# Optimization experiments

Hardware: AMD Instinct MI355X
Metric: run time of the kernel (lower is better)

The kernel has to match this reference:

```python
import jax, jax.numpy as jnp
import numpy as np

IN_FEATURES = 1024
OUT_FEATURES = 256
GRID_SIZE = 5
SPLINE_ORDER = 3
SCALE_BASE = 1.0
GRID_RANGE = (-1.0, 1.0)


def make_grid():
    h = (GRID_RANGE[1] - GRID_RANGE[0]) / GRID_SIZE
    g = jnp.arange(-SPLINE_ORDER, GRID_SIZE + SPLINE_ORDER + 1, dtype=jnp.float32) * h + GRID_RANGE[0]
    # (in_features, grid_size + 2*spline_order + 1) = (1024, 12)
    return jnp.broadcast_to(g[None, :], (IN_FEATURES, g.shape[0]))


def setup_inputs() -> dict:
    key = jax.random.key(0)
    k1, k2, k3 = jax.random.split(key, 3)
    batch = 16384
    x = jax.random.normal(k1, (batch, IN_FEATURES), dtype=jnp.float32)
    base_weight = jax.random.normal(k2, (OUT_FEATURES, IN_FEATURES), dtype=jnp.float32) * 0.03
    n_basis = GRID_SIZE + SPLINE_ORDER  # 8
    spline_weight = (jax.random.uniform(k3, (OUT_FEATURES, IN_FEATURES * n_basis), dtype=jnp.float32) - 0.5) * 0.1 / n_basis
    grid = make_grid()
    return {"x": x, "base_weight": base_weight, "spline_weight": spline_weight, "grid": grid}


def b_splines(x, grid):
    # x: (B, F) -> (B, F, grid_size + spline_order)
    xe = x[:, :, None]  # (B, F, 1)
    bases = ((xe >= grid[:, :-1]) & (xe < grid[:, 1:])).astype(x.dtype)
    for k in range(1, SPLINE_ORDER + 1):
        left = (xe - grid[:, : -(k + 1)]) / (grid[:, k:-1] - grid[:, : -(k + 1)])
        right = (grid[:, k + 1 :] - xe) / (grid[:, k + 1 :] - grid[:, 1:-k])
        bases = left * bases[:, :, :-1] + right * bases[:, :, 1:]
    return bases.reshape(x.shape[0], -1)  # (B, F*(grid_size+spline_order))


def reference(x, base_weight, spline_weight, grid):
    base_out = jax.nn.silu(x) @ (base_weight * SCALE_BASE).T  # (B, out)
    spline_basis = b_splines(x, grid)                          # (B, F*8)
    spline_out = spline_basis @ spline_weight.T                # (B, out)
    return base_out + spline_out
```

## Files before the change

### kernel.cpp

```cpp
#include <hip/hip_runtime.h>
#include <cstdint>
#include <cstddef>

typedef unsigned short u16;
typedef unsigned int   u32;
typedef unsigned long long u64;
typedef __attribute__((ext_vector_type(8))) short short8;
typedef __attribute__((ext_vector_type(4))) float f32x4;

#define M_ROWS 16384
#define N_COLS 256
#define IN_F   1024
#define K_SPL  8192
#define K_TOT  9216
#define NCHUNK 144
#define SPLITK 2
#define CPB    (NCHUNK / SPLITK)

__device__ __forceinline__ u32 f2bf1(float f) {
  u32 u = __float_as_uint(f);
  u += 0x7fffu + ((u >> 16) & 1u);
  return u >> 16;
}
__device__ __forceinline__ u32 pk2(float a, float b) {
  return f2bf1(a) | (f2bf1(b) << 16);
}
__device__ __forceinline__ float silu(float v) {
  return v * __builtin_amdgcn_rcpf(1.f + __expf(-v));
}

__device__ __forceinline__ uint4 basis8(float xv) {
  float u = fmaf(xv, 2.5f, 5.5f);
  int i0 = (int)u;
  float fr = u - (float)i0;
  float fr2 = fr * fr, fr3 = fr2 * fr;
  float om  = 1.f - fr;
  float om3 = om * om * om;
  float w0 = om3 * (1.f / 6.f);
  float w3 = fr3 * (1.f / 6.f);
  float w1 = fmaf(fr3, 0.5f, fmaf(fr2, -1.f, 2.f / 3.f));
  float w2 = fmaf(fr + fr2 - fr3, 0.5f, 1.f / 6.f);
  u64 W = (u64)pk2(w0, w1) | ((u64)pk2(w2, w3) << 32);
  if (!(u >= 0.f && u < 11.f)) W = 0ull;
  int s = (i0 - 3) * 16;
  u64 lo, hi;
  if (s >= 64)      { int r = s - 64; lo = 0ull; hi = (r < 64) ? (W << r) : 0ull; }
  else if (s > 0)   { lo = W << s;    hi = W >> (64 - s); }
  else if (s == 0)  { lo = W;         hi = 0ull; }
  else              { int r = -s;     lo = (r < 64) ? (W >> r) : 0ull; hi = 0ull; }
  uint4 o;
  o.x = (u32)lo; o.y = (u32)(lo >> 32); o.z = (u32)hi; o.w = (u32)(hi >> 32);
  return o;
}

__global__ void pack_weights(const float* __restrict__ bw, const float* __restrict__ sw,
                             u16* __restrict__ Bp) {
  int o  = blockIdx.y;
  int k4 = (blockIdx.x * blockDim.x + threadIdx.x) * 4;
  const float* src = (k4 < K_SPL) ? (sw + (size_t)o * K_SPL + k4)
                                  : (bw + (size_t)o * IN_F + (k4 - K_SPL));
  float a = src[0], b = src[1], c = src[2], d = src[3];
  uint2 v; v.x = pk2(a, b); v.y = pk2(c, d);
  *(uint2*)(Bp + (size_t)o * K_TOT + k4) = v;
}

__global__ __launch_bounds__(512, 4)
void kan_gemm(const float* __restrict__ x, const u16* __restrict__ Bp,
              float* __restrict__ out) {
  __shared__ __align__(16) u16 Bs[2 * 256 * 64];
  __shared__ __align__(16) u16 As[2 * 64 * 64];

  const int tid  = threadIdx.x;
  const int lane = tid & 63;
  const int w    = tid >> 6;
  const int wm   = w & 1;
  const int wn   = w >> 1;

  const int bid  = blockIdx.x;
  const int kid  = bid & 1;
  const int mb   = bid >> 1;
  const int row0 = mb * 64;
  const int cs   = kid * CPB, c1 = cs + CPB;

  f32x4 acc[2][4];
#pragma unroll
  for (int i = 0; i < 2; ++i)
#pragma unroll
    for (int j = 0; j < 4; ++j)
      acc[i][j] = (f32x4){0.f, 0.f, 0.f, 0.f};

  const int sr = tid >> 3;
  const int sq = tid & 7;

  const int lm = lane & 15;
  const int kg = lane >> 4;
  int a_off[2][2], b_off[2][4];
#pragma unroll
  for (int h = 0; h < 2; ++h) {
    int c = h * 4 + kg;
#pragma unroll
    for (int i = 0; i < 2; ++i) {
      int ra = wm * 32 + i * 16 + lm;
      a_off[h][i] = ra * 64 + ((c ^ (ra & 7)) * 8);
    }
#pragma unroll
    for (int j = 0; j < 4; ++j) {
      int rb = wn * 64 + j * 16 + lm;
      b_off[h][j] = rb * 64 + ((c ^ (rb & 7)) * 8);
    }
  }

  float px;
  float4 pb0, pb1;

  auto LOADX = [&](int c) {
    if (c < 128) {
      px = x[(size_t)(row0 + sr) * IN_F + c * 8 + sq];
    } else {
      const float* xp = x + (size_t)(row0 + sr) * IN_F + (c - 128) * 64 + sq * 8;
      pb0 = *(const float4*)xp;
      pb1 = *(const float4*)(xp + 4);
    }
  };

  auto BUILD = [&](int c, int buf) {
    uint4 q;
    if (c < 128) {
      q = basis8(px);
    } else {
      q.x = pk2(silu(pb0.x), silu(pb0.y));
      q.y = pk2(silu(pb0.z), silu(pb0.w));
      q.z = pk2(silu(pb1.x), silu(pb1.y));
      q.w = pk2(silu(pb1.z), silu(pb1.w));
    }
    *(uint4*)(As + buf * (64 * 64) + sr * 64 + ((sq ^ (sr & 7)) * 8)) = q;
  };

  auto STAGEB = [&](int c, int buf) {
    u16* base = Bs + buf * (256 * 64);
#pragma unroll
    for (int it = 0; it < 4; ++it) {
      int s = tid + it * 512;
      int r_ = s >> 3, cc = (s & 7) ^ (r_ & 7);
      const u16* gp = Bp + (size_t)r_ * K_TOT + c * 64 + cc * 8;
      __builtin_amdgcn_global_load_lds((const __attribute__((address_space(1))) void*)gp,
                                       (__attribute__((address_space(3))) void*)(base + s * 8),
                                       16, 0, 0);
    }
  };

  auto MFMA_PHASE = [&](int buf) {
    const u16* Ab = As + buf * (64 * 64);
    const u16* Bb = Bs + buf * (256 * 64);
#pragma unroll
    for (int h = 0; h < 2; ++h) {
      short8 af[2], bf[4];
#pragma unroll
      for (int i = 0; i < 2; ++i) af[i] = *(const short8*)(Ab + a_off[h][i]);
#pragma unroll
      for (int j = 0; j < 4; ++j) bf[j] = *(const short8*)(Bb + b_off[h][j]);
#pragma unroll
      for (int i = 0; i < 2; ++i)
#pragma unroll
        for (int j = 0; j < 4; ++j)
          acc[i][j] = __builtin_amdgcn_mfma_f32_16x16x32_bf16(af[i], bf[j], acc[i][j], 0, 0, 0);
    }
  };

  LOADX(cs);
  STAGEB(cs, 0);
  BUILD(cs, 0);
  if (cs + 1 < c1) LOADX(cs + 1);
  __syncthreads();

  for (int c = cs; c < c1; c += 2) {
    if (c + 1 < c1) { STAGEB(c + 1, 1); BUILD(c + 1, 1); }
    if (c + 2 < c1) LOADX(c + 2);
    MFMA_PHASE(0);
    __syncthreads();

    if (c + 1 < c1) {
      if (c + 2 < c1) { STAGEB(c + 2, 0); BUILD(c + 2, 0); }
      if (c + 3 < c1) LOADX(c + 3);
      MFMA_PHASE(1);
      __syncthreads();
    }
  }

  const int lc = lane & 15;
  const int lr = (lane >> 4) * 4;
#pragma unroll
  for (int i = 0; i < 2; ++i) {
#pragma unroll
    for (int j = 0; j < 4; ++j) {
      int gr = row0 + wm * 32 + i * 16 + lr;
      int gc = wn * 64 + j * 16 + lc;
      float* po = out + (size_t)gr * N_COLS + gc;
#pragma unroll
      for (int r = 0; r < 4; ++r)
        unsafeAtomicAdd(po + (size_t)r * N_COLS, acc[i][j][r]);
    }
  }
}

extern "C" void kernel_launch(void* const* d_in, const int* in_sizes, int n_in,
                              void* d_out, int out_size, void* d_ws, size_t ws_size,
                              hipStream_t stream) {
  const float* x  = (const float*)d_in[0];
  const float* bw = (const float*)d_in[1];
  const float* sw = (const float*)d_in[2];
  float* out = (float*)d_out;
  u16* Bp = (u16*)d_ws;

  hipMemsetAsync(d_out, 0, (size_t)M_ROWS * N_COLS * sizeof(float), stream);

  dim3 pgrid(K_TOT / 4 / 256, N_COLS);
  pack_weights<<<pgrid, 256, 0, stream>>>(bw, sw, Bp);

  kan_gemm<<<512, 512, 0, stream>>>(x, Bp, out);
}
```

Measured before the change: 204.7 us.

## Halve K chunk to 32, raise split-K to 4, and remap blocks for L2 reuse

Each K chunk shrinks from 64 to 32, which halves the LDS buffers, and split-K goes from 2 to 4, doubling the grid to 1024 blocks. Launch bounds now ask for 8 blocks per CU. The block index is remapped so that groups of 8 M-tiles share one K slice, which is meant to improve L2 reuse of the packed weights. Only half the threads now build A tiles. The aim is more occupancy and parallelism, at the cost of twice as many atomic adds to the output, more barriers per unit of work, and register pressure from the tighter launch bounds.

```diff
diff --git a/kernel.cpp b/kernel.cpp
--- a/kernel.cpp
+++ b/kernel.cpp
@@ -13,8 +13,8 @@
 #define IN_F   1024
 #define K_SPL  8192
 #define K_TOT  9216
-#define NCHUNK 144
-#define SPLITK 2
+#define NCHUNK 288
+#define SPLITK 4
 #define CPB    (NCHUNK / SPLITK)
 
 __device__ __forceinline__ u32 f2bf1(float f) {
@@ -64,11 +64,11 @@
   *(uint2*)(Bp + (size_t)o * K_TOT + k4) = v;
 }
 
-__global__ __launch_bounds__(512, 4)
+__global__ __launch_bounds__(512, 8)
 void kan_gemm(const float* __restrict__ x, const u16* __restrict__ Bp,
               float* __restrict__ out) {
-  __shared__ __align__(16) u16 Bs[2 * 256 * 64];
-  __shared__ __align__(16) u16 As[2 * 64 * 64];
+  __shared__ __align__(16) u16 Bs[2 * 256 * 32];
+  __shared__ __align__(16) u16 As[2 * 64 * 32];
 
   const int tid  = threadIdx.x;
   const int lane = tid & 63;
@@ -76,9 +76,9 @@
   const int wm   = w & 1;
   const int wn   = w >> 1;
 
-  const int bid  = blockIdx.x;
-  const int kid  = bid & 1;
-  const int mb   = bid >> 1;
+  const int p    = blockIdx.x;
+  const int kid  = (p >> 3) & 3;
+  const int mb   = (p & 7) + ((p >> 5) << 3);
   const int row0 = mb * 64;
   const int cs   = kid * CPB, c1 = cs + CPB;
 
@@ -89,43 +89,53 @@
     for (int j = 0; j < 4; ++j)
       acc[i][j] = (f32x4){0.f, 0.f, 0.f, 0.f};
 
-  const int sr = tid >> 3;
-  const int sq = tid & 7;
+  const int  br      = tid >> 2;
+  const int  bq      = tid & 3;
+  const bool builder = tid < 256;
+  const int  a_wr    = br * 32 + ((bq ^ ((br >> 1) & 3)) * 8);
 
   const int lm = lane & 15;
   const int kg = lane >> 4;
-  int a_off[2][2], b_off[2][4];
-#pragma unroll
-  for (int h = 0; h < 2; ++h) {
-    int c = h * 4 + kg;
-#pragma unroll
-    for (int i = 0; i < 2; ++i) {
-      int ra = wm * 32 + i * 16 + lm;
-      a_off[h][i] = ra * 64 + ((c ^ (ra & 7)) * 8);
-    }
-#pragma unroll
-    for (int j = 0; j < 4; ++j) {
-      int rb = wn * 64 + j * 16 + lm;
-      b_off[h][j] = rb * 64 + ((c ^ (rb & 7)) * 8);
-    }
+  int a_off[2], b_off[4];
+#pragma unroll
+  for (int i = 0; i < 2; ++i) {
+    int ra = wm * 32 + i * 16 + lm;
+    a_off[i] = ra * 32 + ((kg ^ ((ra >> 1) & 3)) * 8);
+  }
+#pragma unroll
+  for (int j = 0; j < 4; ++j) {
+    int rb = wn * 64 + j * 16 + lm;
+    b_off[j] = rb * 32 + ((kg ^ ((rb >> 1) & 3)) * 8);
+  }
+
+  u32 stage_goff[2];
+  int stage_loff[2];
+#pragma unroll
+  for (int it = 0; it < 2; ++it) {
+    int s  = tid + it * 512;
+    int r_ = s >> 2, cc = s & 3;
+    stage_goff[it] = (u32)r_ * K_TOT + ((cc ^ ((r_ >> 1) & 3)) * 8);
+    stage_loff[it] = s * 8;
   }
 
   float px;
   float4 pb0, pb1;
 
   auto LOADX = [&](int c) {
-    if (c < 128) {
-      px = x[(size_t)(row0 + sr) * IN_F + c * 8 + sq];
+    if (!builder) return;
+    if (c < 256) {
+      px = x[(size_t)(row0 + br) * IN_F + c * 4 + bq];
     } else {
-      const float* xp = x + (size_t)(row0 + sr) * IN_F + (c - 128) * 64 + sq * 8;
+      const float* xp = x + (size_t)(row0 + br) * IN_F + (c - 256) * 32 + bq * 8;
       pb0 = *(const float4*)xp;
       pb1 = *(const float4*)(xp + 4);
     }
   };
 
   auto BUILD = [&](int c, int buf) {
+    if (!builder) return;
     uint4 q;
-    if (c < 128) {
+    if (c < 256) {
       q = basis8(px);
     } else {
       q.x = pk2(silu(pb0.x), silu(pb0.y));
@@ -133,38 +143,33 @@
       q.z = pk2(silu(pb1.x), silu(pb1.y));
       q.w = pk2(silu(pb1.z), silu(pb1.w));
     }
-    *(uint4*)(As + buf * (64 * 64) + sr * 64 + ((sq ^ (sr & 7)) * 8)) = q;
+    *(uint4*)(As + buf * (64 * 32) + a_wr) = q;
   };
 
   auto STAGEB = [&](int c, int buf) {
-    u16* base = Bs + buf * (256 * 64);
-#pragma unroll
-    for (int it = 0; it < 4; ++it) {
-      int s = tid + it * 512;
-      int r_ = s >> 3, cc = (s & 7) ^ (r_ & 7);
-      const u16* gp = Bp + (size_t)r_ * K_TOT + c * 64 + cc * 8;
+    u16* base = Bs + buf * (256 * 32);
+#pragma unroll
+    for (int it = 0; it < 2; ++it) {
+      const u16* gp = Bp + stage_goff[it] + c * 32;
       __builtin_amdgcn_global_load_lds((const __attribute__((address_space(1))) void*)gp,
-                                       (__attribute__((address_space(3))) void*)(base + s * 8),
+                                       (__attribute__((address_space(3))) void*)(base + stage_loff[it]),
                                        16, 0, 0);
     }
   };
 
   auto MFMA_PHASE = [&](int buf) {
-    const u16* Ab = As + buf * (64 * 64);
-    const u16* Bb = Bs + buf * (256 * 64);
-#pragma unroll
-    for (int h = 0; h < 2; ++h) {
-      short8 af[2], bf[4];
-#pragma unroll
-      for (int i = 0; i < 2; ++i) af[i] = *(const short8*)(Ab + a_off[h][i]);
-#pragma unroll
-      for (int j = 0; j < 4; ++j) bf[j] = *(const short8*)(Bb + b_off[h][j]);
-#pragma unroll
-      for (int i = 0; i < 2; ++i)
-#pragma unroll
-        for (int j = 0; j < 4; ++j)
-          acc[i][j] = __builtin_amdgcn_mfma_f32_16x16x32_bf16(af[i], bf[j], acc[i][j], 0, 0, 0);
-    }
+    const u16* Ab = As + buf * (64 * 32);
+    const u16* Bb = Bs + buf * (256 * 32);
+    short8 af[2], bf[4];
+#pragma unroll
+    for (int i = 0; i < 2; ++i) af[i] = *(const short8*)(Ab + a_off[i]);
+#pragma unroll
+    for (int j = 0; j < 4; ++j) bf[j] = *(const short8*)(Bb + b_off[j]);
+#pragma unroll
+    for (int i = 0; i < 2; ++i)
+#pragma unroll
+      for (int j = 0; j < 4; ++j)
+        acc[i][j] = __builtin_amdgcn_mfma_f32_16x16x32_bf16(af[i], bf[j], acc[i][j], 0, 0, 0);
   };
 
   LOADX(cs);
@@ -217,5 +222,5 @@
   dim3 pgrid(K_TOT / 4 / 256, N_COLS);
   pack_weights<<<pgrid, 256, 0, stream>>>(bw, sw, Bp);
 
-  kan_gemm<<<512, 512, 0, stream>>>(x, Bp, out);
-}
+  kan_gemm<<<1024, 512, 0, stream>>>(x, Bp, out);
+}
```

After: 385.7 us. 1.88x slower.

## Double block to 1024 threads with 16x64 per-wave tiles and split A-build groups

Applied to the files above, without the earlier changes.

Doubles the GEMM block from 512 to 1024 threads, so each of the 16 waves computes a 16x64 output tile instead of 32x64. A-tile building is split by chunk parity between the two 512-thread halves, and the B staging offsets are precomputed. The aim is more resident waves per CU to hide load and basis-build latency. In exchange, each A/B fragment is reused across fewer MFMAs, which raises LDS read traffic per MFMA. The launch bound of (1024, 8) also caps registers per thread and could cause spills.

```diff
diff --git a/kernel.cpp b/kernel.cpp
--- a/kernel.cpp
+++ b/kernel.cpp
@@ -64,7 +64,7 @@
   *(uint2*)(Bp + (size_t)o * K_TOT + k4) = v;
 }
 
-__global__ __launch_bounds__(512, 4)
+__global__ __launch_bounds__(1024, 8)
 void kan_gemm(const float* __restrict__ x, const u16* __restrict__ Bp,
               float* __restrict__ out) {
   __shared__ __align__(16) u16 Bs[2 * 256 * 64];
@@ -73,8 +73,8 @@
   const int tid  = threadIdx.x;
   const int lane = tid & 63;
   const int w    = tid >> 6;
-  const int wm   = w & 1;
-  const int wn   = w >> 1;
+  const int wm   = w & 3;
+  const int wn   = w >> 2;
 
   const int bid  = blockIdx.x;
   const int kid  = bid & 1;
@@ -82,38 +82,40 @@
   const int row0 = mb * 64;
   const int cs   = kid * CPB, c1 = cs + CPB;
 
-  f32x4 acc[2][4];
-#pragma unroll
-  for (int i = 0; i < 2; ++i)
-#pragma unroll
-    for (int j = 0; j < 4; ++j)
-      acc[i][j] = (f32x4){0.f, 0.f, 0.f, 0.f};
-
-  const int sr = tid >> 3;
-  const int sq = tid & 7;
+  f32x4 acc[4];
+#pragma unroll
+  for (int j = 0; j < 4; ++j) acc[j] = (f32x4){0.f, 0.f, 0.f, 0.f};
+
+  const int sr   = (tid >> 3) & 63;
+  const int sq   = tid & 7;
+  const int bgrp = tid >> 9;
 
   const int lm = lane & 15;
   const int kg = lane >> 4;
-  int a_off[2][2], b_off[2][4];
-#pragma unroll
-  for (int h = 0; h < 2; ++h) {
-    int c = h * 4 + kg;
-#pragma unroll
-    for (int i = 0; i < 2; ++i) {
-      int ra = wm * 32 + i * 16 + lm;
-      a_off[h][i] = ra * 64 + ((c ^ (ra & 7)) * 8);
-    }
-#pragma unroll
-    for (int j = 0; j < 4; ++j) {
-      int rb = wn * 64 + j * 16 + lm;
-      b_off[h][j] = rb * 64 + ((c ^ (rb & 7)) * 8);
-    }
+  const int ra = wm * 16 + lm;
+  const int a_base = ra * 64 + ((kg ^ (ra & 7)) * 8);
+  int b_base[4];
+#pragma unroll
+  for (int j = 0; j < 4; ++j) {
+    int rb = wn * 64 + j * 16 + lm;
+    b_base[j] = rb * 64 + ((kg ^ (rb & 7)) * 8);
+  }
+
+  u32 stage_goff[2];
+  int stage_loff[2];
+#pragma unroll
+  for (int it = 0; it < 2; ++it) {
+    int s  = tid + it * 1024;
+    int r_ = s >> 3, cc = (s & 7) ^ (r_ & 7);
+    stage_goff[it] = (u32)r_ * K_TOT + cc * 8;
+    stage_loff[it] = s * 8;
   }
 
   float px;
   float4 pb0, pb1;
 
   auto LOADX = [&](int c) {
+    if ((c & 1) != bgrp) return;
     if (c < 128) {
       px = x[(size_t)(row0 + sr) * IN_F + c * 8 + sq];
     } else {
@@ -124,6 +126,7 @@
   };
 
   auto BUILD = [&](int c, int buf) {
+    if ((c & 1) != bgrp) return;
     uint4 q;
     if (c < 128) {
       q = basis8(px);
@@ -139,12 +142,10 @@
   auto STAGEB = [&](int c, int buf) {
     u16* base = Bs + buf * (256 * 64);
 #pragma unroll
-    for (int it = 0; it < 4; ++it) {
-      int s = tid + it * 512;
-      int r_ = s >> 3, cc = (s & 7) ^ (r_ & 7);
-      const u16* gp = Bp + (size_t)r_ * K_TOT + c * 64 + cc * 8;
+    for (int it = 0; it < 2; ++it) {
+      const u16* gp = Bp + stage_goff[it] + c * 64;
       __builtin_amdgcn_global_load_lds((const __attribute__((address_space(1))) void*)gp,
-                                       (__attribute__((address_space(3))) void*)(base + s * 8),
+                                       (__attribute__((address_space(3))) void*)(base + stage_loff[it]),
                                        16, 0, 0);
     }
   };
@@ -154,16 +155,14 @@
     const u16* Bb = Bs + buf * (256 * 64);
 #pragma unroll
     for (int h = 0; h < 2; ++h) {
-      short8 af[2], bf[4];
-#pragma unroll
-      for (int i = 0; i < 2; ++i) af[i] = *(const short8*)(Ab + a_off[h][i]);
-#pragma unroll
-      for (int j = 0; j < 4; ++j) bf[j] = *(const short8*)(Bb + b_off[h][j]);
-#pragma unroll
-      for (int i = 0; i < 2; ++i)
-#pragma unroll
-        for (int j = 0; j < 4; ++j)
-          acc[i][j] = __builtin_amdgcn_mfma_f32_16x16x32_bf16(af[i], bf[j], acc[i][j], 0, 0, 0);
+      const int hx = h * 32;
+      short8 af = *(const short8*)(Ab + (a_base ^ hx));
+      short8 bf[4];
+#pragma unroll
+      for (int j = 0; j < 4; ++j) bf[j] = *(const short8*)(Bb + (b_base[j] ^ hx));
+#pragma unroll
+      for (int j = 0; j < 4; ++j)
+        acc[j] = __builtin_amdgcn_mfma_f32_16x16x32_bf16(af, bf[j], acc[j], 0, 0, 0);
     }
   };
 
@@ -190,16 +189,13 @@
   const int lc = lane & 15;
   const int lr = (lane >> 4) * 4;
 #pragma unroll
-  for (int i = 0; i < 2; ++i) {
-#pragma unroll
-    for (int j = 0; j < 4; ++j) {
-      int gr = row0 + wm * 32 + i * 16 + lr;
-      int gc = wn * 64 + j * 16 + lc;
-      float* po = out + (size_t)gr * N_COLS + gc;
-#pragma unroll
-      for (int r = 0; r < 4; ++r)
-        unsafeAtomicAdd(po + (size_t)r * N_COLS, acc[i][j][r]);
-    }
+  for (int j = 0; j < 4; ++j) {
+    int gr = row0 + wm * 16 + lr;
+    int gc = wn * 64 + j * 16 + lc;
+    float* po = out + (size_t)gr * N_COLS + gc;
+#pragma unroll
+    for (int r = 0; r < 4; ++r)
+      unsafeAtomicAdd(po + (size_t)r * N_COLS, acc[j][r]);
   }
 }
 
@@ -217,5 +213,5 @@
   dim3 pgrid(K_TOT / 4 / 256, N_COLS);
   pack_weights<<<pgrid, 256, 0, stream>>>(bw, sw, Bp);
 
-  kan_gemm<<<512, 512, 0, stream>>>(x, Bp, out);
-}
+  kan_gemm<<<512, 1024, 0, stream>>>(x, Bp, out);
+}
```

Result: no change. 204.9 us (+0.1%).
